# Performance work log

Measured on AMD Instinct MI355X. Metric: run time of the kernel, lower is better.

The kernel has to match this reference:

```python
import jax, jax.numpy as jnp
import numpy as np
from jax import lax

B, C, H, W = 32, 3, 128, 128
NUM_CLASSES = 101
H2, W2 = H // 2, W // 2
N = H2 * W2                      # 4096 graph nodes


def _grid_graph(h, w):
    """4-neighbor bidirectional grid graph + self loops, with GCN sym-norm coeffs."""
    idx = np.arange(h * w).reshape(h, w)
    src = np.concatenate([idx[:, :-1].ravel(), idx[:, 1:].ravel(),
                          idx[:-1, :].ravel(), idx[1:, :].ravel()])
    dst = np.concatenate([idx[:, 1:].ravel(), idx[:, :-1].ravel(),
                          idx[1:, :].ravel(), idx[:-1, :].ravel()])
    # GCNConv default: add self loops, then D^{-1/2} (A+I) D^{-1/2}
    loop = np.arange(h * w)
    src = np.concatenate([src, loop])
    dst = np.concatenate([dst, loop])
    deg = np.bincount(dst, minlength=h * w).astype(np.float32)
    dinv = 1.0 / np.sqrt(deg)
    norm = dinv[src] * dinv[dst]
    return src.astype(np.int32), dst.astype(np.int32), norm.astype(np.float32)


def setup_inputs() -> dict:
    key = jax.random.key(0)
    ks = jax.random.split(key, 9)
    x = jax.random.normal(ks[0], (B, C, H, W), dtype=jnp.float32)
    conv_w = jax.random.normal(ks[1], (32, C, 3, 3), dtype=jnp.float32) * 0.1
    conv_b = jax.random.normal(ks[2], (32,), dtype=jnp.float32) * 0.01
    gcn_w = jax.random.normal(ks[3], (32, 64), dtype=jnp.float32) * 0.15
    gcn_b = jax.random.normal(ks[4], (64,), dtype=jnp.float32) * 0.01
    fc1_w = jax.random.normal(ks[5], (128, 64 * N), dtype=jnp.float32) * (1.0 / 512.0)
    fc1_b = jax.random.normal(ks[6], (128,), dtype=jnp.float32) * 0.01
    fc2_w = jax.random.normal(ks[7], (NUM_CLASSES, 128), dtype=jnp.float32) * 0.08
    fc2_b = jax.random.normal(ks[8], (NUM_CLASSES,), dtype=jnp.float32) * 0.01
    return {"x": x, "conv_w": conv_w, "conv_b": conv_b, "gcn_w": gcn_w,
            "gcn_b": gcn_b, "fc1_w": fc1_w, "fc1_b": fc1_b,
            "fc2_w": fc2_w, "fc2_b": fc2_b}


def reference(x, conv_w, conv_b, gcn_w, gcn_b, fc1_w, fc1_b, fc2_w, fc2_b):
    # conv1 (3x3, pad=1) + relu + maxpool 2x2
    y = lax.conv_general_dilated(x, conv_w, (1, 1), "SAME",
                                 dimension_numbers=("NCHW", "OIHW", "NCHW"))
    y = jax.nn.relu(y + conv_b[None, :, None, None])
    y = lax.reduce_window(y, -jnp.inf, lax.max, (1, 1, 2, 2), (1, 1, 2, 2), "VALID")
    b, c, h2, w2 = y.shape  # [B, 32, 64, 64]

    # faithful torch x.view(B, -1, 32): raw row-major reinterpretation (NOT transpose)
    xg = y.reshape(b, -1, c)  # [B, N, 32]

    # GCNConv(32 -> 64): linear, then gather -> normalize -> scatter-add
    hfeat = jnp.einsum("bnf,fo->bno", xg, gcn_w)  # [B, N, 64]
    src, dst, norm = _grid_graph(h2, w2)
    src = jnp.asarray(src); dst = jnp.asarray(dst)
    coeff = jnp.asarray(norm, hfeat.dtype)[None, :, None]
    msgs = hfeat[:, src, :] * coeff                      # edge-wise gather
    agg = jnp.zeros_like(hfeat).at[:, dst, :].add(msgs)  # scatter-add
    g = jax.nn.relu(agg + gcn_b)

    # flatten + FCs
    flat = g.reshape(b, -1)  # [B, 64*N]
    f1 = jax.nn.relu(flat @ fc1_w.T + fc1_b)
    return f1 @ fc2_w.T + fc2_b
```

## Files before the change

### kernel.cpp

```cpp
#include <hip/hip_runtime.h>


#define K_FC 262144

__global__ __launch_bounds__(256) void k_conv_pool(
    const float* __restrict__ x, const float* __restrict__ cw,
    const float* __restrict__ cb, float* __restrict__ y)
{
    __shared__ float wl[864];
    __shared__ float tin[3 * 34 * 36];

    int blk = blockIdx.x;
    int b = blk >> 4;
    int tile = blk & 15;
    int ph0 = (tile >> 2) << 4;
    int pw0 = (tile & 3) << 4;
    int t = threadIdx.x;

    for (int i = t; i < 864; i += 256) wl[i] = cw[i];

    int r0 = ph0 * 2 - 1;
    int c0 = pw0 * 2 - 1;
    for (int i = t; i < 3 * 34 * 34; i += 256) {
        int ci = i / 1156;
        int rem = i - ci * 1156;
        int yy = rem / 34;
        int xx = rem - yy * 34;
        int gr = r0 + yy, gc = c0 + xx;
        float v = 0.f;
        if (gr >= 0 && gr < 128 && gc >= 0 && gc < 128)
            v = x[((b * 3 + ci) * 128 + gr) * 128 + gc];
        tin[ci * 1224 + yy * 36 + xx] = v;
    }
    __syncthreads();

    int ph = t >> 4, pw = t & 15;
    float p[3][4][4];
#pragma unroll
    for (int ci = 0; ci < 3; ++ci)
#pragma unroll
        for (int dy = 0; dy < 4; ++dy) {
            const float2* row = (const float2*)&tin[ci * 1224 + (2 * ph + dy) * 36 + 2 * pw];
            float2 v0 = row[0], v1 = row[1];
            p[ci][dy][0] = v0.x; p[ci][dy][1] = v0.y;
            p[ci][dy][2] = v1.x; p[ci][dy][3] = v1.y;
        }

    int obase = (b * 32 * 64 + (ph0 + ph)) * 64 + pw0 + pw;
    for (int co = 0; co < 32; ++co) {
        float s00 = 0.f, s01 = 0.f, s10 = 0.f, s11 = 0.f;
#pragma unroll
        for (int ci = 0; ci < 3; ++ci)
#pragma unroll
            for (int ky = 0; ky < 3; ++ky)
#pragma unroll
                for (int kx = 0; kx < 3; ++kx) {
                    float wv = wl[co * 27 + ci * 9 + ky * 3 + kx];
                    s00 = fmaf(p[ci][ky][kx],         wv, s00);
                    s01 = fmaf(p[ci][ky][kx + 1],     wv, s01);
                    s10 = fmaf(p[ci][ky + 1][kx],     wv, s10);
                    s11 = fmaf(p[ci][ky + 1][kx + 1], wv, s11);
                }
        float m = fmaxf(fmaxf(s00, s01), fmaxf(s10, s11)) + cb[co];
        y[obase + co * 4096] = fmaxf(m, 0.f);
    }
}

__device__ __forceinline__ float dinvf(int h, int w) {
    int d = 1 + (w > 0) + (w < 63) + (h > 0) + (h < 63);
    return rsqrtf((float)d);
}

__device__ __forceinline__ void acc4(const float* __restrict__ yb, int hq, int wq,
                                     int fh, float c,
                                     float4& a0, float4& a1, float4& a2, float4& a3)
{
    const float4* s = (const float4*)(yb + (((hq << 6) + wq) << 5) + fh);
    float4 v0 = s[0], v1 = s[1], v2 = s[2], v3 = s[3];
    a0.x = fmaf(c, v0.x, a0.x); a0.y = fmaf(c, v0.y, a0.y);
    a0.z = fmaf(c, v0.z, a0.z); a0.w = fmaf(c, v0.w, a0.w);
    a1.x = fmaf(c, v1.x, a1.x); a1.y = fmaf(c, v1.y, a1.y);
    a1.z = fmaf(c, v1.z, a1.z); a1.w = fmaf(c, v1.w, a1.w);
    a2.x = fmaf(c, v2.x, a2.x); a2.y = fmaf(c, v2.y, a2.y);
    a2.z = fmaf(c, v2.z, a2.z); a2.w = fmaf(c, v2.w, a2.w);
    a3.x = fmaf(c, v3.x, a3.x); a3.y = fmaf(c, v3.y, a3.y);
    a3.z = fmaf(c, v3.z, a3.z); a3.w = fmaf(c, v3.w, a3.w);
}

__global__ __launch_bounds__(256) void k_gcn(
    const float* __restrict__ y, const float* __restrict__ gw,
    const float* __restrict__ gb, float* __restrict__ g)
{
    __shared__ float zl[128 * 36];

    int blk = blockIdx.x;
    int b = blk >> 5;
    int r = blk & 31;
    int t = threadIdx.x;
    const float* yb = y + b * 131072;

    int lane = t & 63;
    int wave = t >> 6;
    float wreg[32];
#pragma unroll
    for (int f = 0; f < 32; ++f) wreg[f] = gw[f * 64 + lane];
    float bias = gb[lane];

    {
        int l = t >> 1;
        int fh = (t & 1) << 4;
        int h = 2 * r + (l >> 6);
        int w = l & 63;
        float dp = dinvf(h, w);
        float4 a0 = {0,0,0,0}, a1 = {0,0,0,0}, a2 = {0,0,0,0}, a3 = {0,0,0,0};
        acc4(yb, h, w, fh, dp * dp, a0, a1, a2, a3);
        if (w > 0)  acc4(yb, h, w - 1, fh, dp * dinvf(h, w - 1), a0, a1, a2, a3);
        if (w < 63) acc4(yb, h, w + 1, fh, dp * dinvf(h, w + 1), a0, a1, a2, a3);
        if (h > 0)  acc4(yb, h - 1, w, fh, dp * dinvf(h - 1, w), a0, a1, a2, a3);
        if (h < 63) acc4(yb, h + 1, w, fh, dp * dinvf(h + 1, w), a0, a1, a2, a3);
        float4* zrow = (float4*)&zl[l * 36 + fh];
        zrow[0] = a0; zrow[1] = a1; zrow[2] = a2; zrow[3] = a3;
    }
    __syncthreads();

    int l0 = wave << 5;
    int pbase = r * 128;
    float* gout = g + (size_t)b * 262144;
    for (int n = 0; n < 32; ++n) {
        int l = l0 + n;
        const float4* zz = (const float4*)&zl[l * 36];
        float acc = bias;
#pragma unroll
        for (int f4 = 0; f4 < 8; ++f4) {
            float4 zv = zz[f4];
            acc = fmaf(zv.x, wreg[f4 * 4 + 0], acc);
            acc = fmaf(zv.y, wreg[f4 * 4 + 1], acc);
            acc = fmaf(zv.z, wreg[f4 * 4 + 2], acc);
            acc = fmaf(zv.w, wreg[f4 * 4 + 3], acc);
        }
        gout[(pbase + l) * 64 + lane] = fmaxf(acc, 0.f);
    }
}

__global__ __launch_bounds__(256, 4) void k_fc1(
    const float* __restrict__ flat, const float* __restrict__ w,
    float* __restrict__ partial)
{
    __shared__ float Wl[128 * 36];
    __shared__ float Al[32 * 36];

    int t = threadIdx.x;
    int blk = blockIdx.x;
    int k0 = blk << 8;

    int sub = t >> 7;
    int tt = t & 127;
    int bg = tt >> 4;
    int b0 = bg << 2;
    int jg = tt & 15;

    int jb  = t >> 3;
    int kq4 = (t & 7) << 2;
    const float* wsrc = w    + (size_t)jb * K_FC + k0 + kq4;
    const float* asrc = flat + (size_t)jb * K_FC + k0 + kq4;
    float* wdst = &Wl[jb * 36 + kq4];
    float* adst = &Al[jb * 36 + kq4];

    float acc[4][8];
#pragma unroll
    for (int i = 0; i < 4; ++i)
#pragma unroll
        for (int jj = 0; jj < 8; ++jj) acc[i][jj] = 0.f;

    float4 pw0 = *(const float4*)(wsrc);
    float4 pw1 = *(const float4*)(wsrc + (size_t)32 * K_FC);
    float4 pw2 = *(const float4*)(wsrc + (size_t)64 * K_FC);
    float4 pw3 = *(const float4*)(wsrc + (size_t)96 * K_FC);
    float4 pa  = *(const float4*)(asrc);

    for (int s = 0; s < 8; ++s) {
        *(float4*)(wdst)           = pw0;
        *(float4*)(wdst + 32 * 36) = pw1;
        *(float4*)(wdst + 64 * 36) = pw2;
        *(float4*)(wdst + 96 * 36) = pw3;
        *(float4*)(adst)           = pa;
        __syncthreads();

        if (s < 7) {
            int ks = (s + 1) << 5;
            pw0 = *(const float4*)(wsrc + ks);
            pw1 = *(const float4*)(wsrc + (size_t)32 * K_FC + ks);
            pw2 = *(const float4*)(wsrc + (size_t)64 * K_FC + ks);
            pw3 = *(const float4*)(wsrc + (size_t)96 * K_FC + ks);
            pa  = *(const float4*)(asrc + ks);
        }

#pragma unroll
        for (int c = 0; c < 4; ++c) {
            int kk = (sub << 4) + (c << 2);
            float4 av[4];
#pragma unroll
            for (int i = 0; i < 4; ++i)
                av[i] = *(const float4*)&Al[(b0 + i) * 36 + kk];
#pragma unroll
            for (int jj = 0; jj < 8; ++jj) {
                float4 wv = *(const float4*)&Wl[(jg + (jj << 4)) * 36 + kk];
#pragma unroll
                for (int i = 0; i < 4; ++i) {
                    acc[i][jj] = fmaf(av[i].x, wv.x, acc[i][jj]);
                    acc[i][jj] = fmaf(av[i].y, wv.y, acc[i][jj]);
                    acc[i][jj] = fmaf(av[i].z, wv.z, acc[i][jj]);
                    acc[i][jj] = fmaf(av[i].w, wv.w, acc[i][jj]);
                }
            }
        }
        __syncthreads();
    }

    if (sub == 1) {
#pragma unroll
        for (int i = 0; i < 4; ++i)
#pragma unroll
            for (int jj = 0; jj < 8; ++jj)
                Wl[((i << 3) + jj) * 128 + tt] = acc[i][jj];
    }
    __syncthreads();
    if (sub == 0) {
        float* pout = partial + ((size_t)blk << 12);
#pragma unroll
        for (int i = 0; i < 4; ++i)
#pragma unroll
            for (int jj = 0; jj < 8; ++jj)
                pout[(b0 + i) * 128 + jg + (jj << 4)] =
                    acc[i][jj] + Wl[((i << 3) + jj) * 128 + tt];
    }
}

__global__ __launch_bounds__(256) void k_red(
    const float* __restrict__ partial, float* __restrict__ f1)
{
    __shared__ float4 Sl[256];
    int t = threadIdx.x;
    int e4 = (blockIdx.x << 2) + (t & 3);
    int ng = t >> 2;
    const float4* p = (const float4*)partial;
    float4 a = {0.f, 0.f, 0.f, 0.f};
#pragma unroll
    for (int i = 0; i < 16; ++i) {
        int ns = ng + (i << 6);
        float4 v = p[(size_t)ns * 1024 + e4];
        a.x += v.x; a.y += v.y; a.z += v.z; a.w += v.w;
    }
    Sl[t] = a;
    __syncthreads();
    for (int off = 128; off >= 4; off >>= 1) {
        if (t < off) {
            float4 u = Sl[t], v = Sl[t + off];
            u.x += v.x; u.y += v.y; u.z += v.z; u.w += v.w;
            Sl[t] = u;
        }
        __syncthreads();
    }
    if (t < 4) ((float4*)f1)[(blockIdx.x << 2) + t] = Sl[t];
}

__global__ __launch_bounds__(256) void k_fc2(
    const float* __restrict__ f1, const float* __restrict__ b1,
    const float* __restrict__ w2, const float* __restrict__ b2,
    float* __restrict__ out)
{
    int idx = blockIdx.x * 256 + threadIdx.x;
    if (idx >= 32 * 101) return;
    int b = idx / 101;
    int c = idx - b * 101;
    const float4* fp = (const float4*)(f1 + b * 128);
    const float4* bp = (const float4*)b1;
    const float4* wp = (const float4*)(w2 + c * 128);
    float acc = b2[c];
#pragma unroll
    for (int q = 0; q < 32; ++q) {
        float4 f = fp[q], bb = bp[q], ww = wp[q];
        acc = fmaf(fmaxf(f.x + bb.x, 0.f), ww.x, acc);
        acc = fmaf(fmaxf(f.y + bb.y, 0.f), ww.y, acc);
        acc = fmaf(fmaxf(f.z + bb.z, 0.f), ww.z, acc);
        acc = fmaf(fmaxf(f.w + bb.w, 0.f), ww.w, acc);
    }
    out[idx] = acc;
}

extern "C" void kernel_launch(void* const* d_in, const int* in_sizes, int n_in,
                              void* d_out, int out_size, void* d_ws, size_t ws_size,
                              hipStream_t stream)
{
    const float* x  = (const float*)d_in[0];
    const float* cw = (const float*)d_in[1];
    const float* cb = (const float*)d_in[2];
    const float* gw = (const float*)d_in[3];
    const float* gb = (const float*)d_in[4];
    const float* w1 = (const float*)d_in[5];
    const float* b1 = (const float*)d_in[6];
    const float* w2 = (const float*)d_in[7];
    const float* b2 = (const float*)d_in[8];
    float* out = (float*)d_out;

    float* y       = (float*)d_ws;
    float* g       = y + 4194304;
    float* partial = g + 8388608;
    float* f1      = partial + 4194304;

    k_conv_pool<<<512, 256, 0, stream>>>(x, cw, cb, y);
    k_gcn<<<1024, 256, 0, stream>>>(y, gw, gb, g);
    k_fc1<<<1024, 256, 0, stream>>>(g, w1, partial);
    k_red<<<256, 256, 0, stream>>>(partial, f1);
    k_fc2<<<13, 256, 0, stream>>>(f1, b1, w2, b2, out);
}
```

Baseline: 295.0 us.

## Load fc1 weights directly from global into registers, double-buffer activations

The fc1 split-K kernel no longer stages the 128x32 weight tile through LDS. Each thread now reads its weight float4s straight from global memory, since every weight element is used by only one thread group. The activation tile is double-buffered in LDS so only one barrier per step remains, and a separate LDS buffer holds the final reduction. The risk is less coalesced global weight access, because each thread touches 8 rows at stride K, and global load latency now sits directly in the FMA loop.

```diff
diff --git a/kernel.cpp b/kernel.cpp
--- a/kernel.cpp
+++ b/kernel.cpp
@@ -146,8 +146,8 @@
     const float* __restrict__ flat, const float* __restrict__ w,
     float* __restrict__ partial)
 {
-    __shared__ float Wl[128 * 36];
-    __shared__ float Al[32 * 36];
+    __shared__ float Al[2][32 * 36];
+    __shared__ float Rl[32 * 128];
 
     int t = threadIdx.x;
     int blk = blockIdx.x;
@@ -159,12 +159,15 @@
     int b0 = bg << 2;
     int jg = tt & 15;
 
+    const float* wp[8];
+#pragma unroll
+    for (int jj = 0; jj < 8; ++jj)
+        wp[jj] = w + (size_t)(jg + (jj << 4)) * K_FC + k0 + (sub << 4);
+
     int jb  = t >> 3;
     int kq4 = (t & 7) << 2;
-    const float* wsrc = w    + (size_t)jb * K_FC + k0 + kq4;
     const float* asrc = flat + (size_t)jb * K_FC + k0 + kq4;
-    float* wdst = &Wl[jb * 36 + kq4];
-    float* adst = &Al[jb * 36 + kq4];
+    int adst = jb * 36 + kq4;
 
     float acc[4][8];
 #pragma unroll
@@ -172,39 +175,29 @@
 #pragma unroll
         for (int jj = 0; jj < 8; ++jj) acc[i][jj] = 0.f;
 
-    float4 pw0 = *(const float4*)(wsrc);
-    float4 pw1 = *(const float4*)(wsrc + (size_t)32 * K_FC);
-    float4 pw2 = *(const float4*)(wsrc + (size_t)64 * K_FC);
-    float4 pw3 = *(const float4*)(wsrc + (size_t)96 * K_FC);
-    float4 pa  = *(const float4*)(asrc);
+    {
+        float4 v = *(const float4*)(asrc);
+        *(float4*)&Al[0][adst] = v;
+    }
+    __syncthreads();
 
     for (int s = 0; s < 8; ++s) {
-        *(float4*)(wdst)           = pw0;
-        *(float4*)(wdst + 32 * 36) = pw1;
-        *(float4*)(wdst + 64 * 36) = pw2;
-        *(float4*)(wdst + 96 * 36) = pw3;
-        *(float4*)(adst)           = pa;
-        __syncthreads();
-
-        if (s < 7) {
-            int ks = (s + 1) << 5;
-            pw0 = *(const float4*)(wsrc + ks);
-            pw1 = *(const float4*)(wsrc + (size_t)32 * K_FC + ks);
-            pw2 = *(const float4*)(wsrc + (size_t)64 * K_FC + ks);
-            pw3 = *(const float4*)(wsrc + (size_t)96 * K_FC + ks);
-            pa  = *(const float4*)(asrc + ks);
-        }
-
+        int cur = s & 1;
+        float4 pa;
+        if (s < 7) pa = *(const float4*)(asrc + ((s + 1) << 5));
+
+        const float* al = &Al[cur][0];
+        int soff = s << 5;
 #pragma unroll
         for (int c = 0; c < 4; ++c) {
             int kk = (sub << 4) + (c << 2);
             float4 av[4];
 #pragma unroll
             for (int i = 0; i < 4; ++i)
-                av[i] = *(const float4*)&Al[(b0 + i) * 36 + kk];
+                av[i] = *(const float4*)&al[(b0 + i) * 36 + kk];
 #pragma unroll
             for (int jj = 0; jj < 8; ++jj) {
-                float4 wv = *(const float4*)&Wl[(jg + (jj << 4)) * 36 + kk];
+                float4 wv = *(const float4*)(wp[jj] + soff + (c << 2));
 #pragma unroll
                 for (int i = 0; i < 4; ++i) {
                     acc[i][jj] = fmaf(av[i].x, wv.x, acc[i][jj]);
@@ -214,6 +207,7 @@
                 }
             }
         }
+        if (s < 7) *(float4*)&Al[cur ^ 1][adst] = pa;
         __syncthreads();
     }
 
@@ -222,7 +216,7 @@
         for (int i = 0; i < 4; ++i)
 #pragma unroll
             for (int jj = 0; jj < 8; ++jj)
-                Wl[((i << 3) + jj) * 128 + tt] = acc[i][jj];
+                Rl[((i << 3) + jj) * 128 + tt] = acc[i][jj];
     }
     __syncthreads();
     if (sub == 0) {
@@ -232,7 +226,7 @@
 #pragma unroll
             for (int jj = 0; jj < 8; ++jj)
                 pout[(b0 + i) * 128 + jg + (jj << 4)] =
-                    acc[i][jj] + Wl[((i << 3) + jj) * 128 + tt];
+                    acc[i][jj] + Rl[((i << 3) + jj) * 128 + tt];
     }
 }
 
```

After: 401.5 us. 36.1% more time.
